# Performance work log

Hardware: AMD Instinct MI355X
Metric: run time of the kernel (lower is better)

Reference implementation:

```python
import jax, jax.numpy as jnp
import numpy as np

B, Q, K, A, H, C, O = 32, 512, 512, 256, 8, 32, 256  # batch, queries, keys, channels, heads, head_dim, out_dim


def setup_inputs() -> dict:
    key = jax.random.key(0)
    ks = jax.random.split(key, 12)
    s = 0.02
    return {
        "q_data": jax.random.normal(ks[0], (B, Q, A), jnp.float32),
        "m_data": jax.random.normal(ks[1], (B, K, A), jnp.float32),
        "bias": jax.random.normal(ks[2], (B, 1, 1, K), jnp.float32),
        "nonbatched_bias": jax.random.normal(ks[3], (H, Q, K), jnp.float32),
        "batched_bias": jax.random.normal(ks[4], (B, H, Q, K), jnp.float32),
        "query_w": jax.random.normal(ks[5], (A, H, C), jnp.float32) * s,
        "key_w": jax.random.normal(ks[6], (A, H, C), jnp.float32) * s,
        "value_w": jax.random.normal(ks[7], (A, H, C), jnp.float32) * s,
        "gating_w": jax.random.normal(ks[8], (A, H, C), jnp.float32) * s,
        "gating_b": jnp.ones((H, C), jnp.float32),
        "output_w": jax.random.normal(ks[9], (H, C, O), jnp.float32) * s,
        "output_b": jnp.zeros((O,), jnp.float32),
    }


def reference(q_data, m_data, bias, nonbatched_bias, batched_bias,
              query_w, key_w, value_w, gating_w, gating_b, output_w, output_b):
    key_scale = query_w.shape[-1] ** -0.5
    q = jnp.einsum('bqa,ahc->bqhc', q_data, query_w) * key_scale
    k = jnp.einsum('bka,ahc->bkhc', m_data, key_w)
    v = jnp.einsum('bka,ahc->bkhc', m_data, value_w)
    logits = jnp.einsum('bqhc,bkhc->bhqk', q, k) + bias
    logits = logits + nonbatched_bias[None] + batched_bias
    weights = jax.nn.softmax(logits, axis=-1)
    weighted_avg = jnp.einsum('bhqk,bkhc->bqhc', weights, v)
    gate = jax.nn.sigmoid(jnp.einsum('bqc,chv->bqhv', q_data, gating_w) + gating_b)
    weighted_avg = weighted_avg * gate
    return jnp.einsum('bqhc,hco->bqo', weighted_avg, output_w) + output_b
```

## Files before the change

### kernel.cpp

```cpp
#include <hip/hip_runtime.h>
#include <cstdint>
#include <cstddef>


typedef __attribute__((ext_vector_type(8))) short short8;
typedef __attribute__((ext_vector_type(4))) float f32x4;
typedef __attribute__((ext_vector_type(4))) unsigned int u32x4;
typedef __attribute__((ext_vector_type(2))) unsigned int u32x2;

#define DEVFN static __device__ __forceinline__
#define L2E 1.4426950408889634f

DEVFN float b2f(unsigned int bits16) {
  return __builtin_bit_cast(float, bits16 << 16);
}
DEVFN unsigned int pack2(float a, float b) {
  unsigned int r;
  asm("v_cvt_pk_bf16_f32 %0, %1, %2" : "=v"(r) : "v"(a), "v"(b));
  return r;
}
DEVFN f32x4 mfma16(short8 a, short8 b, f32x4 c) {
  return __builtin_amdgcn_mfma_f32_16x16x32_bf16(a, b, c, 0, 0, 0);
}
#define GLOAD_LDS16_NT(gp, lp)                                     \
  __builtin_amdgcn_global_load_lds(                                \
      (const __attribute__((address_space(1))) void*)(gp),         \
      (__attribute__((address_space(3))) void*)(lp), 16, 0, 2)

__global__ __launch_bounds__(256) void wtrans_kernel(
    const float* __restrict__ qw, const float* __restrict__ kw,
    const float* __restrict__ vw, const float* __restrict__ gw,
    const float* __restrict__ ow,
    unsigned short* __restrict__ wtq, unsigned short* __restrict__ wtk,
    unsigned short* __restrict__ wtv, unsigned short* __restrict__ wtg,
    unsigned short* __restrict__ wt3)
{
  const int matid = blockIdx.x >> 4;
  const int tile  = blockIdx.x & 15;
  const float* src = (matid == 0) ? qw : (matid == 1) ? kw : (matid == 2) ? vw
                   : (matid == 3) ? gw : ow;
  unsigned short* dst = (matid == 0) ? wtq : (matid == 1) ? wtk : (matid == 2) ? wtv
                      : (matid == 3) ? wtg : wt3;
  const int tr = (tile >> 2) * 64, tc = (tile & 3) * 64;
  __shared__ unsigned short T[64 * 72];
  const int t = threadIdx.x;
  {
    const int row = t >> 2, cb = (t & 3) * 16;
#pragma unroll
    for (int ii = 0; ii < 4; ++ii) {
      f32x4 v = *(const f32x4*)&src[(size_t)(tr + row) * 256 + tc + cb + ii * 4];
      u32x2 p; p.x = pack2(v.x, v.y); p.y = pack2(v.z, v.w);
      *(u32x2*)&T[row * 72 + cb + ii * 4] = p;
    }
  }
  __syncthreads();
  {
    const int c0 = t >> 2, rb = (t & 3) * 16;
    unsigned short vals[16];
#pragma unroll
    for (int m = 0; m < 16; ++m) vals[m] = T[(rb + m) * 72 + c0];
    u32x4 s0, s1;
    s0.x = (unsigned)vals[0]  | ((unsigned)vals[1]  << 16);
    s0.y = (unsigned)vals[2]  | ((unsigned)vals[3]  << 16);
    s0.z = (unsigned)vals[4]  | ((unsigned)vals[5]  << 16);
    s0.w = (unsigned)vals[6]  | ((unsigned)vals[7]  << 16);
    s1.x = (unsigned)vals[8]  | ((unsigned)vals[9]  << 16);
    s1.y = (unsigned)vals[10] | ((unsigned)vals[11] << 16);
    s1.z = (unsigned)vals[12] | ((unsigned)vals[13] << 16);
    s1.w = (unsigned)vals[14] | ((unsigned)vals[15] << 16);
    unsigned short* dp = &dst[(size_t)(tc + c0) * 256 + tr + rb];
    *(u32x4*)dp = s0;
    *(u32x4*)(dp + 8) = s1;
  }
}

__global__ __launch_bounds__(512, 4) void proj_kernel(
    const float* __restrict__ q_data, const float* __restrict__ m_data,
    const unsigned short* __restrict__ wtq, const unsigned short* __restrict__ wtk,
    const unsigned short* __restrict__ wtv, const unsigned short* __restrict__ wtg,
    const float* __restrict__ gating_b,
    unsigned short* __restrict__ qp, unsigned short* __restrict__ kp,
    unsigned short* __restrict__ vp, unsigned short* __restrict__ gate)
{
  const int bid = blockIdx.x;
  const bool mside = bid >= 256;
  const int r0 = (mside ? bid - 256 : bid) * 64;
  const float* inp = mside ? m_data : q_data;
  __shared__ unsigned short Alds[64 * 264];
  __shared__ unsigned short Wlds[2][256 * 40];
  const int t = threadIdx.x;
  const int lane = t & 63, wave = t >> 6;
  const int l15 = lane & 15, g = lane >> 4;
  const int stripe = wave & 3, nhalf = wave >> 2;

  {
    const int row = t >> 3, cb = (t & 7) * 32;
    const float* ip = &inp[(size_t)(r0 + row) * 256 + cb];
#pragma unroll
    for (int i = 0; i < 4; ++i) {
      f32x4 a0 = *(const f32x4*)&ip[i * 8];
      f32x4 a1 = *(const f32x4*)&ip[i * 8 + 4];
      u32x4 pk;
      pk.x = pack2(a0.x, a0.y); pk.y = pack2(a0.z, a0.w);
      pk.z = pack2(a1.x, a1.y); pk.w = pack2(a1.z, a1.w);
      *(u32x4*)&Alds[row * 264 + cb + i * 8] = pk;
    }
  }

  const unsigned short* wt0 = mside ? wtk : wtq;
  const unsigned short* wt1 = mside ? wtv : wtg;
  const int wrow = t & 255, whalf = t >> 8;

  {
    const u32x4* wsrc = (const u32x4*)&wt0[(size_t)wrow * 256 + whalf * 16];
    u32x4 a = wsrc[0], b = wsrc[1];
    *(u32x4*)&Wlds[0][wrow * 40 + whalf * 16 + 0] = a;
    *(u32x4*)&Wlds[0][wrow * 40 + whalf * 16 + 8] = b;
  }

  f32x4 acc[8];
#pragma unroll
  for (int j = 0; j < 8; ++j) acc[j] = f32x4{0.f, 0.f, 0.f, 0.f};

  const int arow = (stripe * 16 + l15) * 264 + 8 * g;
  const int grow = r0 + stripe * 16 + l15;
  const int ob = grow >> 9, oq = grow & 511;

#pragma unroll
  for (int s = 0; s < 16; ++s) {
    const int p = s & 1;
    __syncthreads();
    u32x4 nw0, nw1;
    if (s < 15) {
      const unsigned short* wt = (s + 1 < 8) ? wt0 : wt1;
      const u32x4* wsrc =
          (const u32x4*)&wt[(size_t)wrow * 256 + ((s + 1) & 7) * 32 + whalf * 16];
      nw0 = wsrc[0]; nw1 = wsrc[1];
    }
    const int ks = s & 7;
    short8 bf = __builtin_bit_cast(short8, *(const u32x4*)&Alds[arow + ks * 32]);
#pragma unroll
    for (int j = 0; j < 8; ++j) {
      short8 wf = __builtin_bit_cast(short8,
          *(const u32x4*)&Wlds[p][((nhalf * 8 + j) * 16 + l15) * 40 + 8 * g]);
      acc[j] = mfma16(wf, bf, acc[j]);
    }
    if (s < 15) {
      *(u32x4*)&Wlds[p ^ 1][wrow * 40 + whalf * 16 + 0] = nw0;
      *(u32x4*)&Wlds[p ^ 1][wrow * 40 + whalf * 16 + 8] = nw1;
    }
    if (s == 7 || s == 15) {
      const int oi = s >> 3;
      const float QS = 0.17677669529663687f * 1.4426950408889634f;
#pragma unroll
      for (int j = 0; j < 8; ++j) {
        const int n0 = (nhalf * 8 + j) * 16 + 4 * g;
        const int h = n0 >> 5, c0 = n0 & 31;
        const size_t idx = ((size_t)(ob * 8 + h) * 512 + oq) * 32 + c0;
        f32x4 v = acc[j];
        if (!mside) {
          if (oi == 0) {
            u32x2 st;
            st.x = pack2(v.x * QS, v.y * QS);
            st.y = pack2(v.z * QS, v.w * QS);
            *(u32x2*)&qp[idx] = st;
          } else {
            f32x4 gb = *(const f32x4*)&gating_b[n0];
            f32x4 gv;
            gv.x = 1.0f / (1.0f + exp2f(-(v.x + gb.x) * L2E));
            gv.y = 1.0f / (1.0f + exp2f(-(v.y + gb.y) * L2E));
            gv.z = 1.0f / (1.0f + exp2f(-(v.z + gb.z) * L2E));
            gv.w = 1.0f / (1.0f + exp2f(-(v.w + gb.w) * L2E));
            u32x2 st;
            st.x = pack2(gv.x, gv.y); st.y = pack2(gv.z, gv.w);
            *(u32x2*)&gate[idx] = st;
          }
        } else {
          u32x2 st;
          st.x = pack2(v.x, v.y); st.y = pack2(v.z, v.w);
          if (oi == 0) *(u32x2*)&kp[idx] = st;
          else         *(u32x2*)&vp[idx] = st;
        }
        acc[j] = f32x4{0.f, 0.f, 0.f, 0.f};
      }
    }
  }
}

__global__ __launch_bounds__(512, 2) void attn_kernel(
    const unsigned short* __restrict__ qp, const unsigned short* __restrict__ kp,
    const unsigned short* __restrict__ vp,
    const float* __restrict__ bias, const float* __restrict__ nbias,
    const float* __restrict__ bbias,
    unsigned short* __restrict__ wa)
{
  const int bid = blockIdx.x;
  const int h = bid & 7;
  const int b = bid >> 3;
  const int bh = bid;
  const int t = threadIdx.x;
  const int lane = t & 63, wave = t >> 6;
  const int l15 = lane & 15, g = lane >> 4;

  __shared__ unsigned short Klds[512 * 32];
  __shared__ unsigned short Vt[32 * 520];
  __shared__ float Bb[2][8192];
  __shared__ float Bk[512];

  const float* bbb_bh = bbias + (size_t)bh * 262144;
  const int qc = lane >> 3, sl = lane & 7;
  const float* wsrc0 = bbb_bh + (size_t)(wave * 32 + qc) * 512 + ((sl ^ qc) << 2);

#pragma unroll
  for (int i = 0; i < 4; ++i)
    GLOAD_LDS16_NT(wsrc0 + i * 4096,      &Bb[0][(wave * 4 + i) * 256]);
#pragma unroll
  for (int i = 0; i < 4; ++i)
    GLOAD_LDS16_NT(wsrc0 + i * 4096 + 32, &Bb[1][(wave * 4 + i) * 256]);

  {
    const int row = t;
    const u32x4* ks = (const u32x4*)&kp[((size_t)bh * 512 + row) * 32];
    u32x4 k0 = ks[0], k1 = ks[1], k2 = ks[2], k3 = ks[3];
    *(u32x4*)&Klds[row * 32 + 0]  = k0;
    *(u32x4*)&Klds[row * 32 + 8]  = k1;
    *(u32x4*)&Klds[row * 32 + 16] = k2;
    *(u32x4*)&Klds[row * 32 + 24] = k3;
    const u32x4* vs = (const u32x4*)&vp[((size_t)bh * 512 + row) * 32];
#pragma unroll
    for (int cc = 0; cc < 4; ++cc) {
      u32x4 vv = vs[cc];
      unsigned int dw0 = vv.x, dw1 = vv.y, dw2 = vv.z, dw3 = vv.w;
      const int c = cc * 8;
      Vt[(c + 0) * 520 + row] = (unsigned short)(dw0 & 0xffff);
      Vt[(c + 1) * 520 + row] = (unsigned short)(dw0 >> 16);
      Vt[(c + 2) * 520 + row] = (unsigned short)(dw1 & 0xffff);
      Vt[(c + 3) * 520 + row] = (unsigned short)(dw1 >> 16);
      Vt[(c + 4) * 520 + row] = (unsigned short)(dw2 & 0xffff);
      Vt[(c + 5) * 520 + row] = (unsigned short)(dw2 >> 16);
      Vt[(c + 6) * 520 + row] = (unsigned short)(dw3 & 0xffff);
      Vt[(c + 7) * 520 + row] = (unsigned short)(dw3 >> 16);
    }
    if (t < 128) {
      f32x4 bv = *(const f32x4*)&bias[(size_t)b * 512 + t * 4];
      bv.x *= L2E; bv.y *= L2E; bv.z *= L2E; bv.w *= L2E;
      *(f32x4*)&Bk[t * 4] = bv;
    }
  }

  const int pib = ((g & 1) << 4) | ((g >> 1) << 3);
  const bool godd = (g & 1) != 0;
  const int sw0 = (g ^ (l15 & 7)) << 2;
  const int sw1 = ((g + 4) ^ (l15 & 7)) << 2;
  const int bq0 = (wave * 32 + l15) * 32;
  const int bq1 = bq0 + 16 * 32;

  f32x4 Cn00, Cn01, Cn10, Cn11;
  {
    const float* nn = nbias + (size_t)h * 262144
                    + (size_t)(wave * 32 + l15) * 512 + 4 * g;
    Cn00 = *(const f32x4*)nn;
    Cn01 = *(const f32x4*)(nn + 16);
    Cn10 = *(const f32x4*)(nn + 16 * 512);
    Cn11 = *(const f32x4*)(nn + 16 * 512 + 16);
  }

  short8 qf0, qf1;
  f32x4 acc[2][2];
  float l_part[2] = {0.f, 0.f};

  __syncthreads();

  for (int tok = 0; tok < 32; ++tok) {
    const int pass = tok >> 4, kt = tok & 15, p = tok & 1;
    const int k0 = kt * 32;

    if (kt == 0) {
      const int qbase = pass * 256 + wave * 32;
      qf0 = __builtin_bit_cast(short8,
          *(const u32x4*)&qp[((size_t)bh * 512 + qbase + l15) * 32 + 8 * g]);
      qf1 = __builtin_bit_cast(short8,
          *(const u32x4*)&qp[((size_t)bh * 512 + qbase + 16 + l15) * 32 + 8 * g]);
#pragma unroll
      for (int ct = 0; ct < 2; ++ct)
#pragma unroll
        for (int qt = 0; qt < 2; ++qt) acc[ct][qt] = f32x4{0.f, 0.f, 0.f, 0.f};
      l_part[0] = 0.f; l_part[1] = 0.f;
    }

    short8 kf0 = __builtin_bit_cast(short8, *(const u32x4*)&Klds[(k0 + l15) * 32 + 8 * g]);
    short8 kf1 = __builtin_bit_cast(short8, *(const u32x4*)&Klds[(k0 + 16 + l15) * 32 + 8 * g]);
    short8 vf0 = __builtin_bit_cast(short8, *(const u32x4*)&Vt[l15 * 520 + k0 + pib]);
    short8 vf1 = __builtin_bit_cast(short8, *(const u32x4*)&Vt[(16 + l15) * 520 + k0 + pib]);
    f32x4 bks0 = *(const f32x4*)&Bk[k0 + 4 * g];
    f32x4 bks1 = *(const f32x4*)&Bk[k0 + 16 + 4 * g];
    const float* bp = Bb[p];
    f32x4 bb00 = *(const f32x4*)&bp[bq0 + sw0];
    f32x4 bb01 = *(const f32x4*)&bp[bq0 + sw1];
    f32x4 bb10 = *(const f32x4*)&bp[bq1 + sw0];
    f32x4 bb11 = *(const f32x4*)&bp[bq1 + sw1];
    asm volatile("s_waitcnt lgkmcnt(0)" ::: "memory");
    __builtin_amdgcn_sched_barrier(0);

    f32x4 Nn00, Nn01, Nn10, Nn11;
    if (tok < 31) {
      const int nt = tok + 1;
      const float* nn = nbias + (size_t)h * 262144
          + (size_t)((nt >> 4) * 256 + wave * 32 + l15) * 512 + (nt & 15) * 32 + 4 * g;
      Nn00 = *(const f32x4*)nn;
      Nn01 = *(const f32x4*)(nn + 16);
      Nn10 = *(const f32x4*)(nn + 16 * 512);
      Nn11 = *(const f32x4*)(nn + 16 * 512 + 16);
    }

    if (tok < 30) {
      const int ft = tok + 2;
      const float* ws = wsrc0 + (size_t)(ft >> 4) * 131072 + (ft & 15) * 32;
#pragma unroll
      for (int i = 0; i < 4; ++i)
        GLOAD_LDS16_NT(ws + (size_t)i * 4096, &Bb[p][(wave * 4 + i) * 256]);
    }

#pragma unroll
    for (int qt = 0; qt < 2; ++qt) {
      f32x4 bb0 = qt ? bb10 : bb00;
      f32x4 bb1 = qt ? bb11 : bb01;
      f32x4 nb0 = qt ? Cn10 : Cn00;
      f32x4 nb1 = qt ? Cn11 : Cn01;
      f32x4 c0 = bb0 * L2E + (nb0 * L2E + bks0);
      f32x4 c1 = bb1 * L2E + (nb1 * L2E + bks1);
      short8 qf = qt ? qf1 : qf0;
      f32x4 s0 = mfma16(kf0, qf, c0);
      f32x4 s1 = mfma16(kf1, qf, c1);
      f32x4 p0, p1;
      p0.x = exp2f(s0.x); p0.y = exp2f(s0.y);
      p0.z = exp2f(s0.z); p0.w = exp2f(s0.w);
      p1.x = exp2f(s1.x); p1.y = exp2f(s1.y);
      p1.z = exp2f(s1.z); p1.w = exp2f(s1.w);
      l_part[qt] += ((p0.x + p0.y) + (p0.z + p0.w)) +
                    ((p1.x + p1.y) + (p1.z + p1.w));
      unsigned int d0 = pack2(p0.x, p0.y), d1 = pack2(p0.z, p0.w);
      unsigned int e0 = pack2(p1.x, p1.y), e1 = pack2(p1.z, p1.w);
      unsigned int pd0 = __shfl_xor(d0, 16, 64), pd1 = __shfl_xor(d1, 16, 64);
      unsigned int pe0 = __shfl_xor(e0, 16, 64), pe1 = __shfl_xor(e1, 16, 64);
      u32x4 pfu;
      pfu.x = godd ? pe0 : d0;
      pfu.y = godd ? pe1 : d1;
      pfu.z = godd ? e0 : pd0;
      pfu.w = godd ? e1 : pd1;
      short8 pf = __builtin_bit_cast(short8, pfu);
      acc[0][qt] = mfma16(vf0, pf, acc[0][qt]);
      acc[1][qt] = mfma16(vf1, pf, acc[1][qt]);
    }

    if (tok < 31) { Cn00 = Nn00; Cn01 = Nn01; Cn10 = Nn10; Cn11 = Nn11; }

    if (tok < 30)       asm volatile("s_waitcnt vmcnt(8)" ::: "memory");
    else if (tok == 30) asm volatile("s_waitcnt vmcnt(4)" ::: "memory");

    if (kt == 15) {
      const int qbase = pass * 256 + wave * 32;
      unsigned short* wab = wa + (size_t)bh * 512 * 32;
#pragma unroll
      for (int qt = 0; qt < 2; ++qt) {
        float l = l_part[qt];
        l += __shfl_xor(l, 16, 64);
        l += __shfl_xor(l, 32, 64);
        const float rl = 1.0f / l;
        const int q = qbase + qt * 16 + l15;
#pragma unroll
        for (int ct = 0; ct < 2; ++ct) {
          f32x4 v = acc[ct][qt];
          u32x2 st;
          st.x = pack2(v.x * rl, v.y * rl);
          st.y = pack2(v.z * rl, v.w * rl);
          *(u32x2*)&wab[q * 32 + ct * 16 + 4 * g] = st;
        }
      }
    }
  }
}

__global__ __launch_bounds__(256, 2) void outp_kernel(
    const unsigned short* __restrict__ wa, const unsigned short* __restrict__ gate,
    const unsigned short* __restrict__ wt3, const float* __restrict__ out_b,
    float* __restrict__ out)
{
  const int r0 = blockIdx.x * 32;
  const int t = threadIdx.x;
  const int lane = t & 63, wave = t >> 6;
  const int l15 = lane & 15, g = lane >> 4;
  const int stripe = wave & 1, half = wave >> 1;
  __shared__ unsigned short Wlds[2][256 * 40];

  const int grow = r0 + stripe * 16 + l15;
  const int b = grow >> 9, q = grow & 511;

  {
    const u32x4* wsrc = (const u32x4*)&wt3[(size_t)t * 256];
    u32x4 a = wsrc[0], bb = wsrc[1], c = wsrc[2], d = wsrc[3];
    *(u32x4*)&Wlds[0][t * 40 + 0]  = a;
    *(u32x4*)&Wlds[0][t * 40 + 8]  = bb;
    *(u32x4*)&Wlds[0][t * 40 + 16] = c;
    *(u32x4*)&Wlds[0][t * 40 + 24] = d;
  }
  size_t aidx = ((size_t)(b * 8 + 0) * 512 + q) * 32 + 8 * g;
  u32x4 cwv = *(const u32x4*)&wa[aidx];
  u32x4 cgv = *(const u32x4*)&gate[aidx];

  f32x4 acc[8];
#pragma unroll
  for (int j = 0; j < 8; ++j) acc[j] = f32x4{0.f, 0.f, 0.f, 0.f};

#pragma unroll
  for (int s = 0; s < 8; ++s) {
    const int p = s & 1;
    __syncthreads();
    u32x4 nw0, nw1, nw2, nw3, nwv, ngv;
    if (s < 7) {
      const u32x4* wsrc = (const u32x4*)&wt3[(size_t)t * 256 + (s + 1) * 32];
      nw0 = wsrc[0]; nw1 = wsrc[1]; nw2 = wsrc[2]; nw3 = wsrc[3];
      const size_t na = ((size_t)(b * 8 + s + 1) * 512 + q) * 32 + 8 * g;
      nwv = *(const u32x4*)&wa[na];
      ngv = *(const u32x4*)&gate[na];
    }
    float f0 = b2f(cwv.x & 0xffff) * b2f(cgv.x & 0xffff);
    float f1 = b2f(cwv.x >> 16)    * b2f(cgv.x >> 16);
    float f2 = b2f(cwv.y & 0xffff) * b2f(cgv.y & 0xffff);
    float f3 = b2f(cwv.y >> 16)    * b2f(cgv.y >> 16);
    float f4 = b2f(cwv.z & 0xffff) * b2f(cgv.z & 0xffff);
    float f5 = b2f(cwv.z >> 16)    * b2f(cgv.z >> 16);
    float f6 = b2f(cwv.w & 0xffff) * b2f(cgv.w & 0xffff);
    float f7 = b2f(cwv.w >> 16)    * b2f(cgv.w >> 16);
    u32x4 au;
    au.x = pack2(f0, f1); au.y = pack2(f2, f3);
    au.z = pack2(f4, f5); au.w = pack2(f6, f7);
    short8 af = __builtin_bit_cast(short8, au);
#pragma unroll
    for (int j = 0; j < 8; ++j) {
      short8 wf = __builtin_bit_cast(short8,
          *(const u32x4*)&Wlds[p][((half * 8 + j) * 16 + l15) * 40 + 8 * g]);
      acc[j] = mfma16(wf, af, acc[j]);
    }
    if (s < 7) {
      *(u32x4*)&Wlds[p ^ 1][t * 40 + 0]  = nw0;
      *(u32x4*)&Wlds[p ^ 1][t * 40 + 8]  = nw1;
      *(u32x4*)&Wlds[p ^ 1][t * 40 + 16] = nw2;
      *(u32x4*)&Wlds[p ^ 1][t * 40 + 24] = nw3;
      cwv = nwv; cgv = ngv;
    }
  }
#pragma unroll
  for (int j = 0; j < 8; ++j) {
    const int o0 = (half * 8 + j) * 16 + 4 * g;
    f32x4 ob4 = *(const f32x4*)&out_b[o0];
    f32x4 v = acc[j] + ob4;
    *(f32x4*)&out[(size_t)grow * 256 + o0] = v;
  }
}

extern "C" void kernel_launch(void* const* d_in, const int* in_sizes, int n_in,
                              void* d_out, int out_size, void* d_ws, size_t ws_size,
                              hipStream_t stream)
{
  const float* q_data   = (const float*)d_in[0];
  const float* m_data   = (const float*)d_in[1];
  const float* bias     = (const float*)d_in[2];
  const float* nbb      = (const float*)d_in[3];
  const float* bbb      = (const float*)d_in[4];
  const float* query_w  = (const float*)d_in[5];
  const float* key_w    = (const float*)d_in[6];
  const float* value_w  = (const float*)d_in[7];
  const float* gating_w = (const float*)d_in[8];
  const float* gating_b = (const float*)d_in[9];
  const float* output_w = (const float*)d_in[10];
  const float* output_b = (const float*)d_in[11];
  float* out = (float*)d_out;

  const size_t QP_B   = (size_t)32 * 8 * 512 * 32 * 2;
  const size_t GATE_B = (size_t)32 * 8 * 512 * 32 * 2;
  const size_t WT_B   = (size_t)256 * 256 * 2;

  char* ws = (char*)d_ws;
  unsigned short* qp  = (unsigned short*)(ws);
  unsigned short* kp  = (unsigned short*)(ws + QP_B);
  unsigned short* vp  = (unsigned short*)(ws + 2 * QP_B);
  unsigned short* wab = (unsigned short*)(ws + 3 * QP_B);
  unsigned short* gat = (unsigned short*)(ws + 4 * QP_B);
  unsigned short* wtq = (unsigned short*)(ws + 4 * QP_B + GATE_B);
  unsigned short* wtk = (unsigned short*)(ws + 4 * QP_B + GATE_B + WT_B);
  unsigned short* wtv = (unsigned short*)(ws + 4 * QP_B + GATE_B + 2 * WT_B);
  unsigned short* wtg = (unsigned short*)(ws + 4 * QP_B + GATE_B + 3 * WT_B);
  unsigned short* wt3 = (unsigned short*)(ws + 4 * QP_B + GATE_B + 4 * WT_B);
  const size_t need = 4 * QP_B + GATE_B + 5 * WT_B;
  if (ws_size < need) return;

  hipLaunchKernelGGL(wtrans_kernel, dim3(80), dim3(256), 0, stream,
                     query_w, key_w, value_w, gating_w, output_w,
                     wtq, wtk, wtv, wtg, wt3);
  hipLaunchKernelGGL(proj_kernel, dim3(512), dim3(512), 0, stream,
                     q_data, m_data, wtq, wtk, wtv, wtg, gating_b,
                     qp, kp, vp, gat);
  hipLaunchKernelGGL(attn_kernel, dim3(256), dim3(512), 0, stream,
                     qp, kp, vp, bias, nbb, bbb, wab);
  hipLaunchKernelGGL(outp_kernel, dim3(512), dim3(256), 0, stream,
                     wab, gat, wt3, output_b, out);
}
```

Baseline: 121.6 us.

## Triple-buffer batched-bias LDS prefetch and stream K fragments from global

Replaces the double-buffered batched_bias LDS staging with three buffers, so the async global-to-LDS loads are issued two tiles further ahead and the vmcnt waits are adjusted to match. The K tile is no longer staged in LDS; each wave register-prefetches its K fragments for the next tile straight from global memory. This frees the LDS that K used to pay for the third bias buffer and is meant to hide more of the bias-load latency. The cost is more outstanding global loads per tile, repeated K reads from L2, and fragile hand-tuned vmcnt counts.

```diff
diff --git a/kernel.cpp b/kernel.cpp
--- a/kernel.cpp
+++ b/kernel.cpp
@@ -202,9 +202,8 @@
   const int lane = t & 63, wave = t >> 6;
   const int l15 = lane & 15, g = lane >> 4;
 
-  __shared__ unsigned short Klds[512 * 32];
   __shared__ unsigned short Vt[32 * 520];
-  __shared__ float Bb[2][8192];
+  __shared__ float Bb[3][8192];
   __shared__ float Bk[512];
 
   const float* bbb_bh = bbias + (size_t)bh * 262144;
@@ -217,15 +216,12 @@
 #pragma unroll
   for (int i = 0; i < 4; ++i)
     GLOAD_LDS16_NT(wsrc0 + i * 4096 + 32, &Bb[1][(wave * 4 + i) * 256]);
+#pragma unroll
+  for (int i = 0; i < 4; ++i)
+    GLOAD_LDS16_NT(wsrc0 + i * 4096 + 64, &Bb[2][(wave * 4 + i) * 256]);
 
   {
     const int row = t;
-    const u32x4* ks = (const u32x4*)&kp[((size_t)bh * 512 + row) * 32];
-    u32x4 k0 = ks[0], k1 = ks[1], k2 = ks[2], k3 = ks[3];
-    *(u32x4*)&Klds[row * 32 + 0]  = k0;
-    *(u32x4*)&Klds[row * 32 + 8]  = k1;
-    *(u32x4*)&Klds[row * 32 + 16] = k2;
-    *(u32x4*)&Klds[row * 32 + 24] = k3;
     const u32x4* vs = (const u32x4*)&vp[((size_t)bh * 512 + row) * 32];
 #pragma unroll
     for (int cc = 0; cc < 4; ++cc) {
@@ -255,6 +251,10 @@
   const int bq0 = (wave * 32 + l15) * 32;
   const int bq1 = bq0 + 16 * 32;
 
+  const unsigned short* kb = kp + (size_t)bh * 16384;
+  u32x4 Kc0 = *(const u32x4*)&kb[(0 + l15) * 32 + 8 * g];
+  u32x4 Kc1 = *(const u32x4*)&kb[(16 + l15) * 32 + 8 * g];
+
   f32x4 Cn00, Cn01, Cn10, Cn11;
   {
     const float* nn = nbias + (size_t)h * 262144
@@ -269,10 +269,12 @@
   f32x4 acc[2][2];
   float l_part[2] = {0.f, 0.f};
 
+  asm volatile("s_waitcnt vmcnt(0)" ::: "memory");
   __syncthreads();
 
+  int pcur = 0;
   for (int tok = 0; tok < 32; ++tok) {
-    const int pass = tok >> 4, kt = tok & 15, p = tok & 1;
+    const int pass = tok >> 4, kt = tok & 15;
     const int k0 = kt * 32;
 
     if (kt == 0) {
@@ -288,13 +290,13 @@
       l_part[0] = 0.f; l_part[1] = 0.f;
     }
 
-    short8 kf0 = __builtin_bit_cast(short8, *(const u32x4*)&Klds[(k0 + l15) * 32 + 8 * g]);
-    short8 kf1 = __builtin_bit_cast(short8, *(const u32x4*)&Klds[(k0 + 16 + l15) * 32 + 8 * g]);
+    short8 kf0 = __builtin_bit_cast(short8, Kc0);
+    short8 kf1 = __builtin_bit_cast(short8, Kc1);
     short8 vf0 = __builtin_bit_cast(short8, *(const u32x4*)&Vt[l15 * 520 + k0 + pib]);
     short8 vf1 = __builtin_bit_cast(short8, *(const u32x4*)&Vt[(16 + l15) * 520 + k0 + pib]);
     f32x4 bks0 = *(const f32x4*)&Bk[k0 + 4 * g];
     f32x4 bks1 = *(const f32x4*)&Bk[k0 + 16 + 4 * g];
-    const float* bp = Bb[p];
+    const float* bp = Bb[pcur];
     f32x4 bb00 = *(const f32x4*)&bp[bq0 + sw0];
     f32x4 bb01 = *(const f32x4*)&bp[bq0 + sw1];
     f32x4 bb10 = *(const f32x4*)&bp[bq1 + sw0];
@@ -303,6 +305,7 @@
     __builtin_amdgcn_sched_barrier(0);
 
     f32x4 Nn00, Nn01, Nn10, Nn11;
+    u32x4 Kn0, Kn1;
     if (tok < 31) {
       const int nt = tok + 1;
       const float* nn = nbias + (size_t)h * 262144
@@ -311,14 +314,17 @@
       Nn01 = *(const f32x4*)(nn + 16);
       Nn10 = *(const f32x4*)(nn + 16 * 512);
       Nn11 = *(const f32x4*)(nn + 16 * 512 + 16);
-    }
-
-    if (tok < 30) {
-      const int ft = tok + 2;
+      const int nk0 = (nt & 15) * 32;
+      Kn0 = *(const u32x4*)&kb[(nk0 + l15) * 32 + 8 * g];
+      Kn1 = *(const u32x4*)&kb[(nk0 + 16 + l15) * 32 + 8 * g];
+    }
+
+    if (tok < 29) {
+      const int ft = tok + 3;
       const float* ws = wsrc0 + (size_t)(ft >> 4) * 131072 + (ft & 15) * 32;
 #pragma unroll
       for (int i = 0; i < 4; ++i)
-        GLOAD_LDS16_NT(ws + (size_t)i * 4096, &Bb[p][(wave * 4 + i) * 256]);
+        GLOAD_LDS16_NT(ws + (size_t)i * 4096, &Bb[pcur][(wave * 4 + i) * 256]);
     }
 
 #pragma unroll
@@ -353,10 +359,14 @@
       acc[1][qt] = mfma16(vf1, pf, acc[1][qt]);
     }
 
-    if (tok < 31) { Cn00 = Nn00; Cn01 = Nn01; Cn10 = Nn10; Cn11 = Nn11; }
-
-    if (tok < 30)       asm volatile("s_waitcnt vmcnt(8)" ::: "memory");
-    else if (tok == 30) asm volatile("s_waitcnt vmcnt(4)" ::: "memory");
+    if (tok < 31) {
+      Cn00 = Nn00; Cn01 = Nn01; Cn10 = Nn10; Cn11 = Nn11;
+      Kc0 = Kn0; Kc1 = Kn1;
+    }
+
+    if (tok <= 28)      asm volatile("s_waitcnt vmcnt(14)" ::: "memory");
+    else if (tok == 29) asm volatile("s_waitcnt vmcnt(10)" ::: "memory");
+    else if (tok == 30) asm volatile("s_waitcnt vmcnt(6)"  ::: "memory");
 
     if (kt == 15) {
       const int qbase = pass * 256 + wave * 32;
@@ -378,6 +388,8 @@
         }
       }
     }
+
+    pcur = (pcur == 2) ? 0 : pcur + 1;
   }
 }
 
```

After: 129.2 us. +6.3%, slower.
